# Optimization experiments

Hardware: AMD Instinct MI355X
Metric: run time of the kernel (lower is better)

The kernel has to match this reference:

```python
import jax, jax.numpy as jnp
import numpy as np

NUM_HEADS = 16
HEAD_DIM = 64  # hidden_size 1024 / 16 heads


def setup_inputs() -> dict:
    key = jax.random.key(0)
    ks = jax.random.split(key, 9)
    B, T, H = 8, 4096, 1024
    s = 1.0 / np.sqrt(H)
    return {
        "hidden_states": jax.random.normal(ks[0], (B, T + 1, H), jnp.float32),
        "cell_state": jax.random.normal(ks[1], (B, H), jnp.float32),
        "Wq": jax.random.normal(ks[2], (H, H), jnp.float32) * s,
        "bq": jax.random.normal(ks[3], (H,), jnp.float32) * 0.02,
        "Wk": jax.random.normal(ks[4], (H, H), jnp.float32) * s,
        "bk": jax.random.normal(ks[5], (H,), jnp.float32) * 0.02,
        "Wv": jax.random.normal(ks[6], (H, H), jnp.float32) * s,
        "bv": jax.random.normal(ks[7], (H,), jnp.float32) * 0.02,
        "attention_mask": jax.random.randint(ks[8], (B, T), 0, 2, jnp.int32),
        "t": T,
    }


def reference(hidden_states, cell_state, Wq, bq, Wk, bk, Wv, bv, attention_mask, t):
    B, _, H = hidden_states.shape
    nh, hd = NUM_HEADS, HEAD_DIM
    # single-query projection: [B, H] -> [B, nh, hd]
    q = (cell_state @ Wq.T + bq).reshape(B, nh, hd)
    # key/value over first t positions: [B, t, H] -> [B, t, nh, hd]
    kv_in = hidden_states[:, :-1]
    k = (kv_in @ Wk.T + bk).reshape(B, t, nh, hd)
    v = (kv_in @ Wv.T + bv).reshape(B, t, nh, hd)
    # GEMV-like scores: [B, nh, t]
    scores = jnp.einsum("bhd,bthd->bht", q, k) / np.sqrt(hd)
    # mask out positions where attention_mask == 0 (intended semantics of
    # inf * eq(mask, 0) in the original, expressed without -inf*0 NaNs)
    mask_add = jnp.where(attention_mask == 0, -jnp.inf, 0.0)[:, None, :]
    probs = jax.nn.softmax(scores + mask_add, axis=-1)
    # dropout is identity in eval mode
    ctx = jnp.einsum("bht,bthd->bhd", probs, v)  # [B, nh, hd]
    return ctx.reshape(B, nh * hd)  # squeeze of [B, 1, H]
```

## Files before the change

### kernel.cpp

```cpp
#include <hip/hip_runtime.h>
#include <math.h>

#define BB 8
#define TT 4096
#define TP1 4097
#define HH 1024
#define NHD 16

__device__ __forceinline__ float dot4(const float4& a, const float4& b) {
  return a.x*b.x + a.y*b.y + a.z*b.z + a.w*b.w;
}

__global__ __launch_bounds__(256) void k_q(const float* __restrict__ cell,
                                           const float* __restrict__ Wq,
                                           const float* __restrict__ bq,
                                           float* __restrict__ qbuf) {
  __shared__ float cs[BB * HH];
  int tid = threadIdx.x;
  #pragma unroll
  for (int m = 0; m < 8; m++) {
    int idx4 = tid + (m << 8);
    ((float4*)cs)[idx4] = ((const float4*)cell)[idx4];
  }
  __syncthreads();
  int jj = tid >> 6, lane = tid & 63;
  int j = blockIdx.x * 4 + jj;
  float acc[BB];
  #pragma unroll
  for (int b = 0; b < BB; b++) acc[b] = 0.f;
  #pragma unroll
  for (int k = 0; k < 4; k++) {
    int i = (k << 8) + (lane << 2);
    float4 w = *(const float4*)&Wq[(size_t)j * HH + i];
    #pragma unroll
    for (int b = 0; b < BB; b++) acc[b] += dot4(w, *(const float4*)&cs[b * HH + i]);
  }
  #pragma unroll
  for (int b = 0; b < BB; b++) {
    acc[b] += __shfl_xor(acc[b], 1);  acc[b] += __shfl_xor(acc[b], 2);
    acc[b] += __shfl_xor(acc[b], 4);  acc[b] += __shfl_xor(acc[b], 8);
    acc[b] += __shfl_xor(acc[b], 16); acc[b] += __shfl_xor(acc[b], 32);
  }
  if (lane == 0) {
    float bqv = bq[j];
    #pragma unroll
    for (int b = 0; b < BB; b++) qbuf[b * HH + j] = 0.125f * (acc[b] + bqv);
  }
}

__global__ __launch_bounds__(256) void k_qwk(const float* __restrict__ qbuf,
                                             const float* __restrict__ Wk,
                                             const float* __restrict__ bk,
                                             float* __restrict__ qWkT,
                                             float* __restrict__ qbk) {
  __shared__ float q_s[BB * 64];
  __shared__ float red[4 * 64 * 9];
  int tid = threadIdx.x;
  int h = blockIdx.x >> 4, ic = blockIdx.x & 15;
  if (tid < 128) {
    int b = tid >> 4, dq = tid & 15;
    ((float4*)q_s)[tid] = ((const float4*)qbuf)[(b << 8) + (h << 4) + dq];
  }
  __syncthreads();
  int dg = tid >> 6, lane = tid & 63;
  int i = (ic << 6) + lane;
  float acc[BB];
  #pragma unroll
  for (int b = 0; b < BB; b++) acc[b] = 0.f;
  #pragma unroll
  for (int dd = 0; dd < 16; dd++) {
    int d = (dg << 4) + dd;
    float wk = Wk[(size_t)((h << 6) + d) * HH + i];
    #pragma unroll
    for (int b = 0; b < BB; b++) acc[b] += q_s[(b << 6) + d] * wk;
  }
  #pragma unroll
  for (int b = 0; b < BB; b++) red[((dg << 6) + lane) * 9 + b] = acc[b];
  __syncthreads();
  #pragma unroll
  for (int r = 0; r < 2; r++) {
    int o = tid + (r << 8);
    int il = o >> 3, b = o & 7;
    float s = 0.f;
    #pragma unroll
    for (int g = 0; g < 4; g++) s += red[((g << 6) + il) * 9 + b];
    qWkT[((size_t)(b << 10) + (ic << 6) + il) * NHD + h] = s;
  }
  if (ic == 0 && tid < 8) {
    float s = 0.f;
    for (int d = 0; d < 64; d++) s += q_s[(tid << 6) + d] * bk[(h << 6) + d];
    qbk[tid * NHD + h] = s;
  }
}

__device__ __forceinline__ void stage_tile(const float* __restrict__ src, float* dst, int tid) {
  #pragma unroll
  for (int m = 0; m < 4; m++) {
    int idx = tid + (m << 8);
    int r = idx >> 4, c4 = idx & 15;
    *(float4*)&dst[r * 68 + (c4 << 2)] = *(const float4*)&src[(size_t)r * HH + (c4 << 2)];
  }
}

__device__ __forceinline__ void compute_chunk(const float* kv_s, const float* __restrict__ qb,
                                              int lane, int w, float* acc) {
  float4 kv[4];
  #pragma unroll
  for (int cq = 0; cq < 4; cq++)
    kv[cq] = *(const float4*)&kv_s[lane * 68 + (w << 4) + (cq << 2)];
  #pragma unroll
  for (int cq = 0; cq < 4; cq++) {
    const float* qp = qb + (cq << 6);
    #pragma unroll
    for (int h = 0; h < NHD; h++)
      acc[h] += kv[cq].x * qp[h] + kv[cq].y * qp[NHD + h] +
                kv[cq].z * qp[2 * NHD + h] + kv[cq].w * qp[3 * NHD + h];
  }
}

__global__ __launch_bounds__(256) void k_scores(const float* __restrict__ hid,
                                                const float* __restrict__ qWkT,
                                                const float* __restrict__ qbk,
                                                const int* __restrict__ mask,
                                                float* __restrict__ probsT,
                                                float* __restrict__ Spart) {
  __shared__ float kv0[64 * 68];
  __shared__ float kv1[64 * 68];
  __shared__ float qbk_s[NHD];
  int tid = threadIdx.x;
  int b = blockIdx.x >> 6, tile = blockIdx.x & 63;
  int t0 = tile << 6;
  if (tid < NHD) qbk_s[tid] = qbk[b * NHD + tid];
  int w = __builtin_amdgcn_readfirstlane(tid >> 6);
  int lane = tid & 63;
  const float* src = hid + ((size_t)(b * TP1) + t0) * HH;
  const float* qB = qWkT + (((size_t)(b << 10) + (w << 4)) << 4);
  float acc[NHD];
  #pragma unroll
  for (int h = 0; h < NHD; h++) acc[h] = 0.f;

  stage_tile(src, kv0, tid);
  __syncthreads();
  for (int cc = 0; cc < 16; cc += 2) {
    stage_tile(src + ((cc + 1) << 6), kv1, tid);
    compute_chunk(kv0, qB + ((cc << 6) << 4), lane, w, acc);
    __syncthreads();
    if (cc + 2 < 16) stage_tile(src + ((cc + 2) << 6), kv0, tid);
    compute_chunk(kv1, qB + (((cc + 1) << 6) << 4), lane, w, acc);
    __syncthreads();
  }

  float* red = kv0;
  float* e_sh = kv1;
  #pragma unroll
  for (int h4 = 0; h4 < 4; h4++)
    *(float4*)&red[((w << 6) + lane) * NHD + (h4 << 2)] =
        make_float4(acc[h4 * 4], acc[h4 * 4 + 1], acc[h4 * 4 + 2], acc[h4 * 4 + 3]);
  __syncthreads();
  int row = tid >> 2, hq = tid & 3;
  float4 s = make_float4(0.f, 0.f, 0.f, 0.f);
  #pragma unroll
  for (int ww = 0; ww < 4; ww++) {
    float4 r = *(const float4*)&red[((ww << 6) + row) * NHD + (hq << 2)];
    s.x += r.x; s.y += r.y; s.z += r.z; s.w += r.w;
  }
  int mk = mask[b * TT + t0 + row];
  float4 e;
  e.x = mk ? __expf(s.x + qbk_s[hq * 4 + 0]) : 0.f;
  e.y = mk ? __expf(s.y + qbk_s[hq * 4 + 1]) : 0.f;
  e.z = mk ? __expf(s.z + qbk_s[hq * 4 + 2]) : 0.f;
  e.w = mk ? __expf(s.w + qbk_s[hq * 4 + 3]) : 0.f;
  *(float4*)&probsT[((size_t)(b * TT + t0 + row)) * NHD + (hq << 2)] = e;
  *(float4*)&e_sh[row * NHD + (hq << 2)] = e;
  __syncthreads();
  if (tid < 64) {
    int g = tid >> 4, h2 = tid & 15;
    float s2 = 0.f;
    #pragma unroll
    for (int j = 0; j < 16; j++) s2 += e_sh[((g + (j << 2)) << 4) + h2];
    s2 += __shfl_xor(s2, 16);
    s2 += __shfl_xor(s2, 32);
    if (tid < 16) Spart[(size_t)((b << 6) + tile) * NHD + h2] = s2;
  }
}

__global__ void k_sinv(const float* __restrict__ Spart, float* __restrict__ Sinv) {
  int tid = threadIdx.x;
  float s = 0.f;
  for (int c = 0; c < 64; c++) s += Spart[(size_t)((tid >> 4) * 64 + c) * NHD + (tid & 15)];
  Sinv[tid] = 1.f / s;
}

__global__ __launch_bounds__(256) void k_ctx(const float* __restrict__ hid,
                                             const float* __restrict__ probsT,
                                             float* __restrict__ ctxin) {
  __shared__ float red2[2][64 * 64];
  int tid = threadIdx.x;
  int b = blockIdx.x >> 6, ic = (blockIdx.x >> 4) & 3, th = blockIdx.x & 15;
  int w = __builtin_amdgcn_readfirstlane(tid >> 6);
  int lane = tid & 63;
  int t0 = (th << 2) + w;
  const float* kvp = hid + (size_t)b * TP1 * HH + (ic << 8) + (lane << 2);
  const float* pb = probsT + ((size_t)(b << 12) + t0) * NHD;
  float4 acc4[NHD];
  #pragma unroll
  for (int h = 0; h < NHD; h++) acc4[h] = make_float4(0.f, 0.f, 0.f, 0.f);
  #pragma unroll 4
  for (int it = 0; it < 64; it++) {
    int t = it << 6;
    float4 kv = *(const float4*)&kvp[(size_t)(t0 + t) * HH];
    const float* pp = pb + (size_t)t * NHD;
    #pragma unroll
    for (int h = 0; h < NHD; h++) {
      float p = pp[h];
      acc4[h].x += kv.x * p; acc4[h].y += kv.y * p;
      acc4[h].z += kv.z * p; acc4[h].w += kv.w * p;
    }
  }
  if (w < 2) {
    #pragma unroll
    for (int h = 0; h < NHD; h++)
      *(float4*)&red2[w][(lane << 6) + (h << 2)] = acc4[h];
  }
  __syncthreads();
  if (w >= 2) {
    #pragma unroll
    for (int h = 0; h < NHD; h++) {
      float4 r = *(const float4*)&red2[w - 2][(lane << 6) + (h << 2)];
      r.x += acc4[h].x; r.y += acc4[h].y; r.z += acc4[h].z; r.w += acc4[h].w;
      *(float4*)&red2[w - 2][(lane << 6) + (h << 2)] = r;
    }
  }
  __syncthreads();
  #pragma unroll
  for (int j = 0; j < 4; j++) {
    int k = tid + (j << 8);
    float4 a = ((const float4*)red2[0])[k];
    float4 c2 = ((const float4*)red2[1])[k];
    int li = k >> 4, h = k & 15;
    float* dst = ctxin + (((size_t)(b << 4) + h) << 10) + (ic << 8) + (li << 2);
    atomicAdd(dst + 0, a.x + c2.x);
    atomicAdd(dst + 1, a.y + c2.y);
    atomicAdd(dst + 2, a.z + c2.z);
    atomicAdd(dst + 3, a.w + c2.w);
  }
}

__global__ __launch_bounds__(256) void k_out(const float* __restrict__ Wv,
                                             const float* __restrict__ bv,
                                             const float* __restrict__ ctxin,
                                             const float* __restrict__ Sinv,
                                             float* __restrict__ out) {
  __shared__ float cs[BB * HH];
  int tid = threadIdx.x;
  int h = blockIdx.x >> 4;
  int j0 = blockIdx.x * 4;
  #pragma unroll
  for (int m = 0; m < 8; m++) {
    int idx4 = tid + (m << 8);
    int b = idx4 >> 8, i4 = idx4 & 255;
    ((float4*)cs)[idx4] = ((const float4*)ctxin)[(((b << 4) + h) << 8) + i4];
  }
  __syncthreads();
  int jj = tid >> 6, lane = tid & 63;
  int j = j0 + jj;
  float acc[BB];
  #pragma unroll
  for (int b = 0; b < BB; b++) acc[b] = 0.f;
  #pragma unroll
  for (int k = 0; k < 4; k++) {
    int i = (k << 8) + (lane << 2);
    float4 w = *(const float4*)&Wv[(size_t)j * HH + i];
    #pragma unroll
    for (int b = 0; b < BB; b++) acc[b] += dot4(w, *(const float4*)&cs[b * HH + i]);
  }
  #pragma unroll
  for (int b = 0; b < BB; b++) {
    acc[b] += __shfl_xor(acc[b], 1);  acc[b] += __shfl_xor(acc[b], 2);
    acc[b] += __shfl_xor(acc[b], 4);  acc[b] += __shfl_xor(acc[b], 8);
    acc[b] += __shfl_xor(acc[b], 16); acc[b] += __shfl_xor(acc[b], 32);
  }
  if (lane == 0) {
    float bvj = bv[j];
    #pragma unroll
    for (int b = 0; b < BB; b++)
      out[b * HH + j] = Sinv[b * NHD + h] * acc[b] + bvj;
  }
}

extern "C" void kernel_launch(void* const* d_in, const int* in_sizes, int n_in,
                              void* d_out, int out_size, void* d_ws, size_t ws_size,
                              hipStream_t stream) {
  const float* hid  = (const float*)d_in[0];
  const float* cell = (const float*)d_in[1];
  const float* Wq   = (const float*)d_in[2];
  const float* bq   = (const float*)d_in[3];
  const float* Wk   = (const float*)d_in[4];
  const float* bk   = (const float*)d_in[5];
  const float* Wv   = (const float*)d_in[6];
  const float* bv   = (const float*)d_in[7];
  const int*  mask  = (const int*)d_in[8];
  float* out = (float*)d_out;

  float* ws = (float*)d_ws;
  float* qbuf    = ws;
  float* qWkT    = ws + 8192;
  float* qbk     = ws + 139264;
  float* probsT  = ws + 139392;
  float* Spart   = ws + 663680;
  float* Sinv    = ws + 671872;
  float* ctxin   = ws + 672000;

  hipMemsetAsync(ctxin, 0, (size_t)BB * NHD * HH * sizeof(float), stream);
  hipLaunchKernelGGL(k_q,      dim3(256), dim3(256), 0, stream, cell, Wq, bq, qbuf);
  hipLaunchKernelGGL(k_qwk,    dim3(256), dim3(256), 0, stream, qbuf, Wk, bk, qWkT, qbk);
  hipLaunchKernelGGL(k_scores, dim3(512), dim3(256), 0, stream, hid, qWkT, qbk, mask, probsT, Spart);
  hipLaunchKernelGGL(k_sinv,   dim3(1),   dim3(128), 0, stream, Spart, Sinv);
  hipLaunchKernelGGL(k_ctx,    dim3(512), dim3(256), 0, stream, hid, probsT, ctxin);
  hipLaunchKernelGGL(k_out,    dim3(256), dim3(256), 0, stream, Wv, bv, ctxin, Sinv, out);
}
```

Baseline: 295.4 us.

## Fuse scores and context accumulation into one tile kernel with partial-sum reduce

Merges the score and context passes so each 64-row tile of hidden states is read once for scores and then re-read (likely from cache) to accumulate exp-weighted context per head into per-tile partials. A separate reduce kernel sums the 64 partials instead of using atomics, and the memset and probs buffer are removed. The score loop also switches to register-staged prefetch of the next chunk. The cost is a large partials buffer (32 MB written and read back) and heavy register pressure from 16 float4 accumulators plus 16 float4 prefetch registers.

```diff
diff --git a/kernel.cpp b/kernel.cpp
--- a/kernel.cpp
+++ b/kernel.cpp
@@ -93,15 +93,6 @@
   }
 }
 
-__device__ __forceinline__ void stage_tile(const float* __restrict__ src, float* dst, int tid) {
-  #pragma unroll
-  for (int m = 0; m < 4; m++) {
-    int idx = tid + (m << 8);
-    int r = idx >> 4, c4 = idx & 15;
-    *(float4*)&dst[r * 68 + (c4 << 2)] = *(const float4*)&src[(size_t)r * HH + (c4 << 2)];
-  }
-}
-
 __device__ __forceinline__ void compute_chunk(const float* kv_s, const float* __restrict__ qb,
                                               int lane, int w, float* acc) {
   float4 kv[4];
@@ -118,14 +109,14 @@
   }
 }
 
-__global__ __launch_bounds__(256) void k_scores(const float* __restrict__ hid,
-                                                const float* __restrict__ qWkT,
-                                                const float* __restrict__ qbk,
-                                                const int* __restrict__ mask,
-                                                float* __restrict__ probsT,
-                                                float* __restrict__ Spart) {
-  __shared__ float kv0[64 * 68];
-  __shared__ float kv1[64 * 68];
+__global__ __launch_bounds__(256) void k_tile(const float* __restrict__ hid,
+                                              const float* __restrict__ qWkT,
+                                              const float* __restrict__ qbk,
+                                              const int* __restrict__ mask,
+                                              float* __restrict__ ctxpart,
+                                              float* __restrict__ Spart) {
+  __shared__ float smem[16 * 1024];
+  __shared__ float e_sh[64 * NHD];
   __shared__ float qbk_s[NHD];
   int tid = threadIdx.x;
   int b = blockIdx.x >> 6, tile = blockIdx.x & 63;
@@ -135,43 +126,71 @@
   int lane = tid & 63;
   const float* src = hid + ((size_t)(b * TP1) + t0) * HH;
   const float* qB = qWkT + (((size_t)(b << 10) + (w << 4)) << 4);
+
+  float* kv0 = smem;
+  float* kv1 = smem + 4352;
+  int r_[4], c_[4];
+  #pragma unroll
+  for (int m = 0; m < 4; m++) { int idx = tid + (m << 8); r_[m] = idx >> 4; c_[m] = idx & 15; }
+
   float acc[NHD];
   #pragma unroll
   for (int h = 0; h < NHD; h++) acc[h] = 0.f;
 
-  stage_tile(src, kv0, tid);
-  __syncthreads();
+  float4 rgA[4], rgB[4];
+  #pragma unroll
+  for (int m = 0; m < 4; m++) rgA[m] = *(const float4*)&src[(size_t)r_[m] * HH + (c_[m] << 2)];
+  #pragma unroll
+  for (int m = 0; m < 4; m++) *(float4*)&kv0[r_[m] * 68 + (c_[m] << 2)] = rgA[m];
+  __syncthreads();
+  #pragma unroll
+  for (int m = 0; m < 4; m++) rgA[m] = *(const float4*)&src[(size_t)r_[m] * HH + 64 + (c_[m] << 2)];
+
   for (int cc = 0; cc < 16; cc += 2) {
-    stage_tile(src + ((cc + 1) << 6), kv1, tid);
-    compute_chunk(kv0, qB + ((cc << 6) << 4), lane, w, acc);
+    if (cc + 2 < 16) {
+      #pragma unroll
+      for (int m = 0; m < 4; m++)
+        rgB[m] = *(const float4*)&src[(size_t)r_[m] * HH + ((cc + 2) << 6) + (c_[m] << 2)];
+    }
+    compute_chunk(kv0, qB + ((size_t)cc << 10), lane, w, acc);
+    #pragma unroll
+    for (int m = 0; m < 4; m++) *(float4*)&kv1[r_[m] * 68 + (c_[m] << 2)] = rgA[m];
     __syncthreads();
-    if (cc + 2 < 16) stage_tile(src + ((cc + 2) << 6), kv0, tid);
-    compute_chunk(kv1, qB + (((cc + 1) << 6) << 4), lane, w, acc);
+    if (cc + 3 < 16) {
+      #pragma unroll
+      for (int m = 0; m < 4; m++)
+        rgA[m] = *(const float4*)&src[(size_t)r_[m] * HH + ((cc + 3) << 6) + (c_[m] << 2)];
+    }
+    compute_chunk(kv1, qB + ((size_t)(cc + 1) << 10), lane, w, acc);
+    if (cc + 2 < 16) {
+      #pragma unroll
+      for (int m = 0; m < 4; m++) *(float4*)&kv0[r_[m] * 68 + (c_[m] << 2)] = rgB[m];
+    }
     __syncthreads();
   }
 
-  float* red = kv0;
-  float* e_sh = kv1;
+  float* red = smem + 8704;
   #pragma unroll
   for (int h4 = 0; h4 < 4; h4++)
     *(float4*)&red[((w << 6) + lane) * NHD + (h4 << 2)] =
         make_float4(acc[h4 * 4], acc[h4 * 4 + 1], acc[h4 * 4 + 2], acc[h4 * 4 + 3]);
   __syncthreads();
-  int row = tid >> 2, hq = tid & 3;
-  float4 s = make_float4(0.f, 0.f, 0.f, 0.f);
-  #pragma unroll
-  for (int ww = 0; ww < 4; ww++) {
-    float4 r = *(const float4*)&red[((ww << 6) + row) * NHD + (hq << 2)];
-    s.x += r.x; s.y += r.y; s.z += r.z; s.w += r.w;
-  }
-  int mk = mask[b * TT + t0 + row];
-  float4 e;
-  e.x = mk ? __expf(s.x + qbk_s[hq * 4 + 0]) : 0.f;
-  e.y = mk ? __expf(s.y + qbk_s[hq * 4 + 1]) : 0.f;
-  e.z = mk ? __expf(s.z + qbk_s[hq * 4 + 2]) : 0.f;
-  e.w = mk ? __expf(s.w + qbk_s[hq * 4 + 3]) : 0.f;
-  *(float4*)&probsT[((size_t)(b * TT + t0 + row)) * NHD + (hq << 2)] = e;
-  *(float4*)&e_sh[row * NHD + (hq << 2)] = e;
+  {
+    int row = tid >> 2, hq = tid & 3;
+    float4 s = make_float4(0.f, 0.f, 0.f, 0.f);
+    #pragma unroll
+    for (int ww = 0; ww < 4; ww++) {
+      float4 r = *(const float4*)&red[((ww << 6) + row) * NHD + (hq << 2)];
+      s.x += r.x; s.y += r.y; s.z += r.z; s.w += r.w;
+    }
+    int mk = mask[b * TT + t0 + row];
+    float4 e;
+    e.x = mk ? __expf(s.x + qbk_s[hq * 4 + 0]) : 0.f;
+    e.y = mk ? __expf(s.y + qbk_s[hq * 4 + 1]) : 0.f;
+    e.z = mk ? __expf(s.z + qbk_s[hq * 4 + 2]) : 0.f;
+    e.w = mk ? __expf(s.w + qbk_s[hq * 4 + 3]) : 0.f;
+    *(float4*)&e_sh[(row << 4) + (hq << 2)] = e;
+  }
   __syncthreads();
   if (tid < 64) {
     int g = tid >> 4, h2 = tid & 15;
@@ -182,6 +201,58 @@
     s2 += __shfl_xor(s2, 32);
     if (tid < 16) Spart[(size_t)((b << 6) + tile) * NHD + h2] = s2;
   }
+
+  float4 tmp[16];
+  #pragma unroll
+  for (int j = 0; j < 16; j++) {
+    int idx = tid + (j << 8);
+    tmp[j] = *(const float4*)&src[(size_t)(idx >> 8) * HH + ((idx & 255) << 2)];
+  }
+  float4 acc4[NHD];
+  #pragma unroll
+  for (int h = 0; h < NHD; h++) acc4[h] = make_float4(0.f, 0.f, 0.f, 0.f);
+
+  for (int s = 0; s < 4; s++) {
+    __syncthreads();
+    #pragma unroll
+    for (int j = 0; j < 16; j++) ((float4*)smem)[tid + (j << 8)] = tmp[j];
+    __syncthreads();
+    if (s < 3) {
+      #pragma unroll
+      for (int j = 0; j < 16; j++) {
+        int idx = tid + (j << 8);
+        tmp[j] = *(const float4*)&src[(size_t)(((s + 1) << 4) + (idx >> 8)) * HH + ((idx & 255) << 2)];
+      }
+    }
+    #pragma unroll
+    for (int r = 0; r < 16; r++) {
+      float4 kv4 = ((const float4*)smem)[(r << 8) + tid];
+      const float* ep = &e_sh[(((s << 4) + r) << 4)];
+      float4 e0 = *(const float4*)&ep[0];
+      float4 e1 = *(const float4*)&ep[4];
+      float4 e2 = *(const float4*)&ep[8];
+      float4 e3 = *(const float4*)&ep[12];
+      acc4[0].x += e0.x*kv4.x; acc4[0].y += e0.x*kv4.y; acc4[0].z += e0.x*kv4.z; acc4[0].w += e0.x*kv4.w;
+      acc4[1].x += e0.y*kv4.x; acc4[1].y += e0.y*kv4.y; acc4[1].z += e0.y*kv4.z; acc4[1].w += e0.y*kv4.w;
+      acc4[2].x += e0.z*kv4.x; acc4[2].y += e0.z*kv4.y; acc4[2].z += e0.z*kv4.z; acc4[2].w += e0.z*kv4.w;
+      acc4[3].x += e0.w*kv4.x; acc4[3].y += e0.w*kv4.y; acc4[3].z += e0.w*kv4.z; acc4[3].w += e0.w*kv4.w;
+      acc4[4].x += e1.x*kv4.x; acc4[4].y += e1.x*kv4.y; acc4[4].z += e1.x*kv4.z; acc4[4].w += e1.x*kv4.w;
+      acc4[5].x += e1.y*kv4.x; acc4[5].y += e1.y*kv4.y; acc4[5].z += e1.y*kv4.z; acc4[5].w += e1.y*kv4.w;
+      acc4[6].x += e1.z*kv4.x; acc4[6].y += e1.z*kv4.y; acc4[6].z += e1.z*kv4.z; acc4[6].w += e1.z*kv4.w;
+      acc4[7].x += e1.w*kv4.x; acc4[7].y += e1.w*kv4.y; acc4[7].z += e1.w*kv4.z; acc4[7].w += e1.w*kv4.w;
+      acc4[8].x += e2.x*kv4.x; acc4[8].y += e2.x*kv4.y; acc4[8].z += e2.x*kv4.z; acc4[8].w += e2.x*kv4.w;
+      acc4[9].x += e2.y*kv4.x; acc4[9].y += e2.y*kv4.y; acc4[9].z += e2.y*kv4.z; acc4[9].w += e2.y*kv4.w;
+      acc4[10].x += e2.z*kv4.x; acc4[10].y += e2.z*kv4.y; acc4[10].z += e2.z*kv4.z; acc4[10].w += e2.z*kv4.w;
+      acc4[11].x += e2.w*kv4.x; acc4[11].y += e2.w*kv4.y; acc4[11].z += e2.w*kv4.z; acc4[11].w += e2.w*kv4.w;
+      acc4[12].x += e3.x*kv4.x; acc4[12].y += e3.x*kv4.y; acc4[12].z += e3.x*kv4.z; acc4[12].w += e3.x*kv4.w;
+      acc4[13].x += e3.y*kv4.x; acc4[13].y += e3.y*kv4.y; acc4[13].z += e3.y*kv4.z; acc4[13].w += e3.y*kv4.w;
+      acc4[14].x += e3.z*kv4.x; acc4[14].y += e3.z*kv4.y; acc4[14].z += e3.z*kv4.z; acc4[14].w += e3.z*kv4.w;
+      acc4[15].x += e3.w*kv4.x; acc4[15].y += e3.w*kv4.y; acc4[15].z += e3.w*kv4.z; acc4[15].w += e3.w*kv4.w;
+    }
+  }
+  float* dst = ctxpart + (((size_t)((b << 6) + tile)) << 14) + (tid << 2);
+  #pragma unroll
+  for (int h = 0; h < NHD; h++) *(float4*)&dst[h << 10] = acc4[h];
 }
 
 __global__ void k_sinv(const float* __restrict__ Spart, float* __restrict__ Sinv) {
@@ -191,59 +262,16 @@
   Sinv[tid] = 1.f / s;
 }
 
-__global__ __launch_bounds__(256) void k_ctx(const float* __restrict__ hid,
-                                             const float* __restrict__ probsT,
-                                             float* __restrict__ ctxin) {
-  __shared__ float red2[2][64 * 64];
-  int tid = threadIdx.x;
-  int b = blockIdx.x >> 6, ic = (blockIdx.x >> 4) & 3, th = blockIdx.x & 15;
-  int w = __builtin_amdgcn_readfirstlane(tid >> 6);
-  int lane = tid & 63;
-  int t0 = (th << 2) + w;
-  const float* kvp = hid + (size_t)b * TP1 * HH + (ic << 8) + (lane << 2);
-  const float* pb = probsT + ((size_t)(b << 12) + t0) * NHD;
-  float4 acc4[NHD];
-  #pragma unroll
-  for (int h = 0; h < NHD; h++) acc4[h] = make_float4(0.f, 0.f, 0.f, 0.f);
-  #pragma unroll 4
-  for (int it = 0; it < 64; it++) {
-    int t = it << 6;
-    float4 kv = *(const float4*)&kvp[(size_t)(t0 + t) * HH];
-    const float* pp = pb + (size_t)t * NHD;
-    #pragma unroll
-    for (int h = 0; h < NHD; h++) {
-      float p = pp[h];
-      acc4[h].x += kv.x * p; acc4[h].y += kv.y * p;
-      acc4[h].z += kv.z * p; acc4[h].w += kv.w * p;
-    }
-  }
-  if (w < 2) {
-    #pragma unroll
-    for (int h = 0; h < NHD; h++)
-      *(float4*)&red2[w][(lane << 6) + (h << 2)] = acc4[h];
-  }
-  __syncthreads();
-  if (w >= 2) {
-    #pragma unroll
-    for (int h = 0; h < NHD; h++) {
-      float4 r = *(const float4*)&red2[w - 2][(lane << 6) + (h << 2)];
-      r.x += acc4[h].x; r.y += acc4[h].y; r.z += acc4[h].z; r.w += acc4[h].w;
-      *(float4*)&red2[w - 2][(lane << 6) + (h << 2)] = r;
-    }
-  }
-  __syncthreads();
-  #pragma unroll
-  for (int j = 0; j < 4; j++) {
-    int k = tid + (j << 8);
-    float4 a = ((const float4*)red2[0])[k];
-    float4 c2 = ((const float4*)red2[1])[k];
-    int li = k >> 4, h = k & 15;
-    float* dst = ctxin + (((size_t)(b << 4) + h) << 10) + (ic << 8) + (li << 2);
-    atomicAdd(dst + 0, a.x + c2.x);
-    atomicAdd(dst + 1, a.y + c2.y);
-    atomicAdd(dst + 2, a.z + c2.z);
-    atomicAdd(dst + 3, a.w + c2.w);
-  }
+__global__ __launch_bounds__(256) void k_reduce(const float* __restrict__ ctxpart,
+                                                float* __restrict__ ctxin) {
+  int tid = threadIdx.x;
+  int b = blockIdx.x >> 6, h = (blockIdx.x >> 2) & 15, qi = blockIdx.x & 3;
+  int i = (qi << 8) + tid;
+  const float* p = ctxpart + ((size_t)((b << 6) * NHD + h) << 10) + i;
+  float s = 0.f;
+  #pragma unroll 8
+  for (int t = 0; t < 64; t++) s += p[(size_t)t << 14];
+  ctxin[(size_t)(((b << 4) + h) << 10) + i] = s;
 }
 
 __global__ __launch_bounds__(256) void k_out(const float* __restrict__ Wv,
@@ -306,16 +334,15 @@
   float* qbuf    = ws;
   float* qWkT    = ws + 8192;
   float* qbk     = ws + 139264;
-  float* probsT  = ws + 139392;
-  float* Spart   = ws + 663680;
-  float* Sinv    = ws + 671872;
-  float* ctxin   = ws + 672000;
-
-  hipMemsetAsync(ctxin, 0, (size_t)BB * NHD * HH * sizeof(float), stream);
+  float* Spart   = ws + 139392;
+  float* Sinv    = ws + 147584;
+  float* ctxin   = ws + 147712;
+  float* ctxpart = ws + 278784;
+
   hipLaunchKernelGGL(k_q,      dim3(256), dim3(256), 0, stream, cell, Wq, bq, qbuf);
   hipLaunchKernelGGL(k_qwk,    dim3(256), dim3(256), 0, stream, qbuf, Wk, bk, qWkT, qbk);
-  hipLaunchKernelGGL(k_scores, dim3(512), dim3(256), 0, stream, hid, qWkT, qbk, mask, probsT, Spart);
+  hipLaunchKernelGGL(k_tile,   dim3(512), dim3(256), 0, stream, hid, qWkT, qbk, mask, ctxpart, Spart);
   hipLaunchKernelGGL(k_sinv,   dim3(1),   dim3(128), 0, stream, Spart, Sinv);
-  hipLaunchKernelGGL(k_ctx,    dim3(512), dim3(256), 0, stream, hid, probsT, ctxin);
+  hipLaunchKernelGGL(k_reduce, dim3(512), dim3(256), 0, stream, ctxpart, ctxin);
   hipLaunchKernelGGL(k_out,    dim3(256), dim3(256), 0, stream, Wv, bv, ctxin, Sinv, out);
 }
```

Result: slower. 421.0 us (+42.5%).
